# Kernel tuning notes

Measured on AMD Instinct MI355X. Metric: run time of the kernel, lower is better.

## Reference

```python
import jax, jax.numpy as jnp
import numpy as np

B, N, DIN, DM, NH = 8, 2048, 256, 256, 4
DK = DM // NH


def setup_inputs() -> dict:
    key = jax.random.key(0)
    ks = jax.random.split(key, 8)
    x = jax.random.normal(ks[0], (B, N, DIN), dtype=jnp.float32)
    # contiguous valid ranges per sample (padding on both ends), matching
    # the module's assumption that torch.where(mask)[0][0]/[−1] define a span
    starts = jax.random.randint(ks[1], (B,), 0, N // 8)
    lens = jax.random.randint(ks[2], (B,), N // 2, N - N // 8)
    pos = jnp.arange(N)
    attention_mask = ((pos[None, :] >= starts[:, None])
                      & (pos[None, :] < starts[:, None] + lens[:, None])).astype(jnp.int32)
    s = 0.02
    Wq = jax.random.normal(ks[3], (DIN, DM), jnp.float32) * s
    Wk = jax.random.normal(ks[4], (DIN, DM), jnp.float32) * s
    Wv = jax.random.normal(ks[5], (DIN, DM), jnp.float32) * s
    Wo = jax.random.normal(ks[6], (DM, DM), jnp.float32) * s
    bq = jnp.zeros((DM,), jnp.float32)
    bk = jnp.zeros((DM,), jnp.float32)
    bv = jnp.zeros((DM,), jnp.float32)
    bo = jnp.zeros((DM,), jnp.float32)
    return {"x": x, "attention_mask": attention_mask,
            "Wq": Wq, "bq": bq, "Wk": Wk, "bk": bk,
            "Wv": Wv, "bv": bv, "Wo": Wo, "bo": bo}


def reference(x, attention_mask, Wq, bq, Wk, bk, Wv, bv, Wo, bo):
    b, n, _ = x.shape
    nh, dk = NH, DK
    scale = 1.0 / np.sqrt(dk)
    q = (x @ Wq + bq).reshape(b, n, nh, dk).transpose(0, 2, 1, 3)  # [b,h,n,dk]
    k = (x @ Wk + bk).reshape(b, n, nh, dk).transpose(0, 2, 1, 3)
    v = (x @ Wv + bv).reshape(b, n, nh, dk).transpose(0, 2, 1, 3)
    dist = jnp.einsum('bhid,bhjd->bhij', q, k) * scale  # [b,h,n,n]

    # Vectorized equivalent of the per-sample python-loop mask:
    # start = first True index; end = last True index (torch slice start:end
    # is EXCLUSIVE of the last valid position -- preserved faithfully).
    m = attention_mask.astype(bool)
    pos = jnp.arange(n)
    start = jnp.argmax(m, axis=1)                      # [b]
    end = n - 1 - jnp.argmax(m[:, ::-1], axis=1)       # [b] last True index
    valid = (pos[None, :] >= start[:, None]) & (pos[None, :] < end[:, None])  # [b,n]
    bias = jnp.where(valid[:, :, None] & valid[:, None, :], 0.0, -1e10)       # [b,n,n]

    dist = jax.nn.softmax(dist + bias[:, None, :, :], axis=-1)
    att = jnp.einsum('bhij,bhjd->bhid', dist, v)       # [b,h,n,dk]
    att = att.transpose(0, 2, 1, 3).reshape(b, n, nh * dk)
    return att @ Wo + bo
```

## Files before the change

kernel.cpp:

```cpp
#include <hip/hip_runtime.h>
#include <hip/hip_bf16.h>
#include <math.h>

namespace {
constexpr int Bb  = 8;
constexpr int Nn  = 2048;
constexpr int DIN_ = 256;
constexpr int DM_  = 256;
constexpr int NH_  = 4;
constexpr int DK_  = 64;
constexpr int BH_  = Bb * NH_;
constexpr float SCALE = 0.125f;
}

typedef __attribute__((ext_vector_type(8))) _Float16 half8;
typedef __attribute__((ext_vector_type(2))) __fp16 fp16x2;
typedef __attribute__((ext_vector_type(4))) float f32x4;

static __device__ __forceinline__ unsigned pkrtz_u32(float a, float b) {
    union { fp16x2 h; unsigned u; } u;
    u.h = __builtin_amdgcn_cvt_pkrtz(a, b);
    return u.u;
}

static __device__ __forceinline__ half8 h8_from_u32x4(unsigned w0, unsigned w1,
                                                      unsigned w2, unsigned w3) {
    union { unsigned u[4]; half8 h; } u;
    u.u[0] = w0; u.u[1] = w1; u.u[2] = w2; u.u[3] = w3;
    return u.h;
}

__global__ __launch_bounds__(256) void prep_kernel(
    const int* __restrict__ mask, int* __restrict__ bounds,
    float* __restrict__ cmsum,
    const float* __restrict__ W0, const float* __restrict__ W1,
    const float* __restrict__ W2, const float* __restrict__ W3,
    _Float16* __restrict__ T0, _Float16* __restrict__ T1,
    _Float16* __restrict__ T2, _Float16* __restrict__ T3)
{
    const int bid = blockIdx.x;
    const int tid = threadIdx.x;
    if (bid < 8) {
        cmsum[bid * 256 + tid] = 0.0f;
        const int b = bid;
        __shared__ int smin[256], smax[256];
        int lmin = Nn, lmax = -1;
        for (int i = tid; i < Nn; i += 256) {
            if (mask[b * Nn + i]) {
                if (i < lmin) lmin = i;
                if (i > lmax) lmax = i;
            }
        }
        smin[tid] = lmin; smax[tid] = lmax;
        __syncthreads();
        for (int s = 128; s > 0; s >>= 1) {
            if (tid < s) {
                smin[tid] = min(smin[tid], smin[tid + s]);
                smax[tid] = max(smax[tid], smax[tid + s]);
            }
            __syncthreads();
        }
        if (tid == 0) { bounds[b * 2] = smin[0]; bounds[b * 2 + 1] = smax[0]; }
    } else {
        const int lin = bid - 8;
        const int wsel = lin >> 6;
        const float* W; _Float16* T;
        switch (wsel) {
            case 0: W = W0; T = T0; break;
            case 1: W = W1; T = T1; break;
            case 2: W = W2; T = T2; break;
            default: W = W3; T = T3; break;
        }
        const int idx = (lin & 63) * 256 + tid;
        const int n = idx & 255;
        const int k0 = (idx >> 8) << 2;
        _Float16 h4[4];
        #pragma unroll
        for (int j = 0; j < 4; ++j) h4[j] = (_Float16)W[(size_t)(k0 + j) * 256 + n];
        *(uint2*)&T[(size_t)n * 256 + k0] = *(const uint2*)h4;
    }
}

__global__ __launch_bounds__(256) void qkv_mfma(
    const float* __restrict__ x,
    const _Float16* __restrict__ Wtq, const float* __restrict__ bq,
    const _Float16* __restrict__ Wtk, const float* __restrict__ bk,
    const _Float16* __restrict__ Wtv, const float* __restrict__ bv,
    _Float16* __restrict__ Qh, _Float16* __restrict__ Kh, _Float16* __restrict__ Vt,
    float* __restrict__ cmsum)
{
    const int zsel = blockIdx.y >> 2;
    const int n0 = (blockIdx.y & 3) * 64;
    const int m0 = blockIdx.x * 128;
    const _Float16* Wt; const float* bias;
    if (zsel == 0)      { Wt = Wtq; bias = bq; }
    else if (zsel == 1) { Wt = Wtk; bias = bk; }
    else                { Wt = Wtv; bias = bv; }

    const int tid = threadIdx.x;
    const int w = tid >> 6, lane = tid & 63;
    const int a = lane & 15, g = lane >> 4;
    const int b = m0 >> 11;

    __shared__ __align__(16) _Float16 As[128 * 64];
    __shared__ __align__(16) _Float16 Bs[64 * 64];

    f32x4 acc[4][2] = {{{0,0,0,0},{0,0,0,0}},{{0,0,0,0},{0,0,0,0}},
                       {{0,0,0,0},{0,0,0,0}},{{0,0,0,0},{0,0,0,0}}};

    for (int step = 0; step < 4; ++step) {
        const int k0 = step * 64;
        {
            const int rb = tid >> 3, fc = tid & 7;
            #pragma unroll
            for (int p = 0; p < 4; ++p) {
                const int row = p * 32 + rb;
                const float4 v0 = *(const float4*)&x[(size_t)(m0 + row) * 256 + k0 + fc * 8];
                const float4 v1 = *(const float4*)&x[(size_t)(m0 + row) * 256 + k0 + fc * 8 + 4];
                _Float16 h[8];
                h[0]=(_Float16)v0.x; h[1]=(_Float16)v0.y; h[2]=(_Float16)v0.z; h[3]=(_Float16)v0.w;
                h[4]=(_Float16)v1.x; h[5]=(_Float16)v1.y; h[6]=(_Float16)v1.z; h[7]=(_Float16)v1.w;
                const int byo = (fc * 16) ^ ((row & 7) << 4);
                *(uint4*)((char*)As + row * 128 + byo) = *(const uint4*)h;
            }
        }
        #pragma unroll
        for (int i = 0; i < 2; ++i) {
            const int f = 2 * w + i;
            const int rowl = f * 8 + (lane >> 3);
            const int byo = ((lane & 7) * 16) ^ ((rowl & 7) << 4);
            const char* src = (const char*)(Wt + (size_t)(n0 + rowl) * 256 + k0) + byo;
            __builtin_amdgcn_global_load_lds(
                (const __attribute__((address_space(1))) void*)src,
                (__attribute__((address_space(3))) void*)((char*)Bs + f * 1024), 16, 0, 0);
        }
        __syncthreads();

        #pragma unroll
        for (int kc = 0; kc < 2; ++kc) {
            half8 xf[2], wf[4];
            #pragma unroll
            for (int tt = 0; tt < 2; ++tt) {
                const int row = 32 * w + 16 * tt + a;
                const int byo = (kc * 64 + g * 16) ^ ((row & 7) << 4);
                xf[tt] = *(const half8*)((const char*)As + row * 128 + byo);
            }
            #pragma unroll
            for (int nf = 0; nf < 4; ++nf) {
                const int row = 16 * nf + a;
                const int byo = (kc * 64 + g * 16) ^ ((row & 7) << 4);
                wf[nf] = *(const half8*)((const char*)Bs + row * 128 + byo);
            }
            if (zsel < 2) {
                #pragma unroll
                for (int nf = 0; nf < 4; ++nf)
                    #pragma unroll
                    for (int tt = 0; tt < 2; ++tt)
                        acc[nf][tt] = __builtin_amdgcn_mfma_f32_16x16x32_f16(wf[nf], xf[tt], acc[nf][tt], 0,0,0);
            } else {
                #pragma unroll
                for (int nf = 0; nf < 4; ++nf)
                    #pragma unroll
                    for (int tt = 0; tt < 2; ++tt)
                        acc[nf][tt] = __builtin_amdgcn_mfma_f32_16x16x32_f16(xf[tt], wf[nf], acc[nf][tt], 0,0,0);
            }
        }
        __syncthreads();
    }

    if (zsel < 2) {
        _Float16* out = zsel ? Kh : Qh;
        #pragma unroll
        for (int nf = 0; nf < 4; ++nf) {
            const int nb = n0 + 16 * nf + 4 * g;
            const f32x4 bi = *(const f32x4*)&bias[nb];
            const int h = nb >> 6, dkb = nb & 63;
            #pragma unroll
            for (int tt = 0; tt < 2; ++tt) {
                const int tok = (m0 + 32 * w + 16 * tt + a) & 2047;
                const f32x4 d = acc[nf][tt];
                _Float16 q4[4];
                q4[0] = (_Float16)(d[0] + bi[0]);
                q4[1] = (_Float16)(d[1] + bi[1]);
                q4[2] = (_Float16)(d[2] + bi[2]);
                q4[3] = (_Float16)(d[3] + bi[3]);
                *(uint2*)&out[(((size_t)(b * NH_ + h)) * Nn + tok) * DK_ + dkb] = *(const uint2*)q4;
            }
        }
    } else {
        const int h = n0 >> 6;
        #pragma unroll
        for (int nf = 0; nf < 4; ++nf) {
            const int n = n0 + 16 * nf + a;
            const float bs = bias[n];
            const int dk = 16 * nf + a;
            float csum = 8.0f * bs;
            #pragma unroll
            for (int tt = 0; tt < 2; ++tt) {
                const int tokb = (m0 + 32 * w + 16 * tt + 4 * g) & 2047;
                const f32x4 d = acc[nf][tt];
                csum += d[0] + d[1] + d[2] + d[3];
                uint2 pk;
                pk.x = pkrtz_u32(d[0] + bs, d[1] + bs);
                pk.y = pkrtz_u32(d[2] + bs, d[3] + bs);
                *(uint2*)&Vt[(((size_t)(b * NH_ + h)) * DK_ + dk) * Nn + tokb] = pk;
            }
            csum += __shfl_xor(csum, 16, 64);
            csum += __shfl_xor(csum, 32, 64);
            if (g == 0)
                atomicAdd(&cmsum[(b * NH_ + h) * DK_ + dk], csum);
        }
    }
}

__global__ __launch_bounds__(256) void flash_mfma(
    const _Float16* __restrict__ Q, const _Float16* __restrict__ K,
    const _Float16* __restrict__ Vt, const int* __restrict__ bounds,
    _Float16* __restrict__ Oh, float* __restrict__ lw)
{
    const int bid = blockIdx.x;
    const int xcd = bid & 7;
    const int rest = bid >> 3;
    const int qb  = rest & 31;
    const int j   = (rest >> 5) & 3;
    const int s   = rest >> 7;
    const int bh  = j * 8 + xcd;
    const int b  = bh >> 2, h = bh & 3;
    const int q0 = qb * 64;
    const int tid  = threadIdx.x;
    const int w    = tid >> 6;
    const int lane = tid & 63;
    const int a = lane & 15, g = lane >> 4;
    const int start = bounds[2 * b], endv = bounds[2 * b + 1];

    if (q0 + 63 < start || q0 >= endv) return;

    __shared__ __align__(16) _Float16 kfr[2][8][512];
    __shared__ __align__(16) _Float16 vfr[2][8][512];

    const _Float16* Qb = Q  + (size_t)bh * Nn * DK_;
    const _Float16* Kb = K  + (size_t)bh * Nn * DK_;
    const _Float16* Vb = Vt + (size_t)bh * DK_ * Nn;

    const int qrow = q0 + 16 * w + a;
    const half8 qf0 = *(const half8*)&Qb[(size_t)qrow * DK_ + 8 * g];
    const half8 qf1 = *(const half8*)&Qb[(size_t)qrow * DK_ + 32 + 8 * g];

    float l_i = 0.0f;
    f32x4 o0 = {0.f,0.f,0.f,0.f}, o1 = {0.f,0.f,0.f,0.f};
    f32x4 o2 = {0.f,0.f,0.f,0.f}, o3 = {0.f,0.f,0.f,0.f};

#define STAGE(cbuf, kt_) do {                                                        \
        _Pragma("unroll")                                                            \
        for (int ff = 0; ff < 2; ++ff) {                                             \
            const int f  = 2 * w + ff;                                               \
            const int tt = f >> 1, cc = f & 1;                                       \
            const _Float16* ks = &Kb[(size_t)((kt_) + 16 * tt + a) * DK_ + 32 * cc + 8 * g]; \
            __builtin_amdgcn_global_load_lds(                                        \
                (const __attribute__((address_space(1))) void*)ks,                   \
                (__attribute__((address_space(3))) void*)&kfr[cbuf][f][0], 16, 0, 0);\
            const _Float16* vs = &Vb[(size_t)(16 * tt + a) * Nn + (kt_) + 32 * cc + 8 * g]; \
            __builtin_amdgcn_global_load_lds(                                        \
                (const __attribute__((address_space(1))) void*)vs,                   \
                (__attribute__((address_space(3))) void*)&vfr[cbuf][f][0], 16, 0, 0);\
        }                                                                            \
    } while (0)

    const int t0 = start >> 6, t1 = (endv + 63) >> 6;
    const int nt = t1 - t0;
    const int n0t = (nt + 1) >> 1;
    const int ts = (s == 0) ? t0 : t0 + n0t;
    const int te = (s == 0) ? t0 + n0t : t1;

    if (ts < te) {
        const int lo = ts * 64, hiend = te * 64;
        int c = 0;
        STAGE(0, lo);

        for (int kt = lo; kt < hiend; kt += 64) {
            const int nxt = kt + 64;
            if (nxt < hiend) {
                STAGE(c ^ 1, nxt);
                asm volatile("s_waitcnt vmcnt(4)" ::: "memory");
            } else {
                asm volatile("s_waitcnt vmcnt(0)" ::: "memory");
            }
            __builtin_amdgcn_s_barrier();

            const _Float16* kf = &kfr[c][0][0];
            const _Float16* vf = &vfr[c][0][0];

            f32x4 st0 = {0.f,0.f,0.f,0.f}, st1 = {0.f,0.f,0.f,0.f};
            f32x4 st2 = {0.f,0.f,0.f,0.f}, st3 = {0.f,0.f,0.f,0.f};
            __builtin_amdgcn_s_setprio(1);
            st0 = __builtin_amdgcn_mfma_f32_16x16x32_f16(*(const half8*)&kf[0*512 + lane*8], qf0, st0, 0,0,0);
            st0 = __builtin_amdgcn_mfma_f32_16x16x32_f16(*(const half8*)&kf[1*512 + lane*8], qf1, st0, 0,0,0);
            st1 = __builtin_amdgcn_mfma_f32_16x16x32_f16(*(const half8*)&kf[2*512 + lane*8], qf0, st1, 0,0,0);
            st1 = __builtin_amdgcn_mfma_f32_16x16x32_f16(*(const half8*)&kf[3*512 + lane*8], qf1, st1, 0,0,0);
            st2 = __builtin_amdgcn_mfma_f32_16x16x32_f16(*(const half8*)&kf[4*512 + lane*8], qf0, st2, 0,0,0);
            st2 = __builtin_amdgcn_mfma_f32_16x16x32_f16(*(const half8*)&kf[5*512 + lane*8], qf1, st2, 0,0,0);
            st3 = __builtin_amdgcn_mfma_f32_16x16x32_f16(*(const half8*)&kf[6*512 + lane*8], qf0, st3, 0,0,0);
            st3 = __builtin_amdgcn_mfma_f32_16x16x32_f16(*(const half8*)&kf[7*512 + lane*8], qf1, st3, 0,0,0);
            __builtin_amdgcn_s_setprio(0);

            float pv[4][4];
            float rsum = 0.0f;
            const bool edge = (kt < start) || (kt + 64 > endv);
            if (edge) {
                #pragma unroll
                for (int t = 0; t < 4; ++t) {
                    const f32x4 sv = (t == 0) ? st0 : (t == 1) ? st1 : (t == 2) ? st2 : st3;
                    #pragma unroll
                    for (int r = 0; r < 4; ++r) {
                        const int col = kt + 16 * t + 4 * g + r;
                        const bool ok = (col >= start) && (col < endv);
                        const float e = ok ? __expf(sv[r] * SCALE) : 0.0f;
                        pv[t][r] = e;
                        rsum += e;
                    }
                }
            } else {
                #pragma unroll
                for (int t = 0; t < 4; ++t) {
                    const f32x4 sv = (t == 0) ? st0 : (t == 1) ? st1 : (t == 2) ? st2 : st3;
                    #pragma unroll
                    for (int r = 0; r < 4; ++r) {
                        const float e = __expf(sv[r] * SCALE);
                        pv[t][r] = e;
                        rsum += e;
                    }
                }
            }
            rsum += __shfl_xor(rsum, 16, 64);
            rsum += __shfl_xor(rsum, 32, 64);
            l_i += rsum;

            unsigned pk[4][2];
            #pragma unroll
            for (int t = 0; t < 4; ++t) {
                pk[t][0] = pkrtz_u32(pv[t][0], pv[t][1]);
                pk[t][1] = pkrtz_u32(pv[t][2], pv[t][3]);
            }
            const int gsel = g >> 1;
            unsigned aw[2][4];
            #pragma unroll
            for (int cq = 0; cq < 2; ++cq) {
                #pragma unroll
                for (int wd = 0; wd < 4; ++wd) {
                    const int srcLane = a + 16 * (2 * (g & 1) + (wd >> 1));
                    const int lo2 = __shfl((int)pk[2 * cq    ][wd & 1], srcLane, 64);
                    const int hi2 = __shfl((int)pk[2 * cq + 1][wd & 1], srcLane, 64);
                    aw[cq][wd] = (unsigned)(gsel ? hi2 : lo2);
                }
            }
            const half8 pa0 = h8_from_u32x4(aw[0][0], aw[0][1], aw[0][2], aw[0][3]);
            const half8 pa1 = h8_from_u32x4(aw[1][0], aw[1][1], aw[1][2], aw[1][3]);

            __builtin_amdgcn_s_setprio(1);
            o0 = __builtin_amdgcn_mfma_f32_16x16x32_f16(pa0, *(const half8*)&vf[0*512 + lane*8], o0, 0,0,0);
            o0 = __builtin_amdgcn_mfma_f32_16x16x32_f16(pa1, *(const half8*)&vf[1*512 + lane*8], o0, 0,0,0);
            o1 = __builtin_amdgcn_mfma_f32_16x16x32_f16(pa0, *(const half8*)&vf[2*512 + lane*8], o1, 0,0,0);
            o1 = __builtin_amdgcn_mfma_f32_16x16x32_f16(pa1, *(const half8*)&vf[3*512 + lane*8], o1, 0,0,0);
            o2 = __builtin_amdgcn_mfma_f32_16x16x32_f16(pa0, *(const half8*)&vf[4*512 + lane*8], o2, 0,0,0);
            o2 = __builtin_amdgcn_mfma_f32_16x16x32_f16(pa1, *(const half8*)&vf[5*512 + lane*8], o2, 0,0,0);
            o3 = __builtin_amdgcn_mfma_f32_16x16x32_f16(pa0, *(const half8*)&vf[6*512 + lane*8], o3, 0,0,0);
            o3 = __builtin_amdgcn_mfma_f32_16x16x32_f16(pa1, *(const half8*)&vf[7*512 + lane*8], o3, 0,0,0);
            __builtin_amdgcn_s_setprio(0);

            asm volatile("" ::: "memory");
            __builtin_amdgcn_s_barrier();
            c ^= 1;
        }
    }
#undef STAGE

    const size_t half = (size_t)Bb * Nn * DM_;
    _Float16* ob = Oh + (size_t)s * half + ((size_t)b * Nn) * DM_ + h * DK_;
    #pragma unroll
    for (int td = 0; td < 4; ++td) {
        const f32x4 ov = (td == 0) ? o0 : (td == 1) ? o1 : (td == 2) ? o2 : o3;
        #pragma unroll
        for (int r = 0; r < 4; ++r) {
            const int qr = q0 + 16 * w + 4 * g + r;
            ob[(size_t)qr * DM_ + 16 * td + a] = (_Float16)ov[r];
        }
    }
    if (g == 0) {
        const int tok = q0 + 16 * w + a;
        lw[(size_t)s * BH_ * Nn + (size_t)bh * Nn + tok] = l_i;
    }
}

__global__ __launch_bounds__(256) void proj_mfma(
    const _Float16* __restrict__ Oh, const float* __restrict__ lw,
    const int* __restrict__ bounds, const float* __restrict__ cmsum,
    const _Float16* __restrict__ Wt, const float* __restrict__ bias,
    float* __restrict__ out)
{
    const int m0 = blockIdx.x * 128;
    const int n0 = blockIdx.y * 64;
    const int tid = threadIdx.x;
    const int w = tid >> 6, lane = tid & 63;
    const int a = lane & 15, g = lane >> 4;
    const int b = m0 >> 11;
    const int start = bounds[2 * b], endv = bounds[2 * b + 1];

    __shared__ __align__(16) _Float16 As[128 * 64];
    __shared__ __align__(16) _Float16 Bs[64 * 64];

    const size_t half = (size_t)Bb * Nn * DM_;

    f32x4 acc[2][4] = {{{0,0,0,0},{0,0,0,0},{0,0,0,0},{0,0,0,0}},
                       {{0,0,0,0},{0,0,0,0},{0,0,0,0},{0,0,0,0}}};

    for (int step = 0; step < 4; ++step) {
        const int k0 = step * 64;
        {
            const int rb = tid >> 3, fc = tid & 7;
            #pragma unroll
            for (int p = 0; p < 4; ++p) {
                const int row = p * 32 + rb;
                const int tok = (m0 + row) & 2047;
                const bool valid = (tok >= start) && (tok < endv);
                const size_t rowoff = ((size_t)b * Nn + tok) * DM_ + k0 + fc * 8;
                _Float16 h[8];
                if (valid) {
                    const int bh = b * NH_ + step;
                    const float l0 = lw[(size_t)bh * Nn + tok];
                    const float l1 = lw[(size_t)BH_ * Nn + (size_t)bh * Nn + tok];
                    const float inv = 1.0f / (l0 + l1);
                    half8 a0 = *(const half8*)&Oh[rowoff];
                    half8 a1 = *(const half8*)&Oh[half + rowoff];
                    #pragma unroll
                    for (int k = 0; k < 8; ++k)
                        h[k] = (_Float16)(((float)a0[k] + (float)a1[k]) * inv);
                } else {
                    const float* cmp = &cmsum[(b * NH_ + step) * DK_ + fc * 8];
                    const float4 c0 = *(const float4*)cmp;
                    const float4 c1 = *(const float4*)(cmp + 4);
                    h[0]=(_Float16)(c0.x*(1.0f/2048.0f)); h[1]=(_Float16)(c0.y*(1.0f/2048.0f));
                    h[2]=(_Float16)(c0.z*(1.0f/2048.0f)); h[3]=(_Float16)(c0.w*(1.0f/2048.0f));
                    h[4]=(_Float16)(c1.x*(1.0f/2048.0f)); h[5]=(_Float16)(c1.y*(1.0f/2048.0f));
                    h[6]=(_Float16)(c1.z*(1.0f/2048.0f)); h[7]=(_Float16)(c1.w*(1.0f/2048.0f));
                }
                const int byo = (fc * 16) ^ ((row & 7) << 4);
                *(uint4*)((char*)As + row * 128 + byo) = *(const uint4*)h;
            }
        }
        #pragma unroll
        for (int i = 0; i < 2; ++i) {
            const int f = 2 * w + i;
            const int rowl = f * 8 + (lane >> 3);
            const int byo = ((lane & 7) * 16) ^ ((rowl & 7) << 4);
            const char* src = (const char*)(Wt + (size_t)(n0 + rowl) * 256 + k0) + byo;
            __builtin_amdgcn_global_load_lds(
                (const __attribute__((address_space(1))) void*)src,
                (__attribute__((address_space(3))) void*)((char*)Bs + f * 1024), 16, 0, 0);
        }
        __syncthreads();

        #pragma unroll
        for (int kc = 0; kc < 2; ++kc) {
            half8 af[2], wf[4];
            #pragma unroll
            for (int tt = 0; tt < 2; ++tt) {
                const int row = 32 * w + 16 * tt + a;
                const int byo = (kc * 64 + g * 16) ^ ((row & 7) << 4);
                af[tt] = *(const half8*)((const char*)As + row * 128 + byo);
            }
            #pragma unroll
            for (int nf = 0; nf < 4; ++nf) {
                const int row = 16 * nf + a;
                const int byo = (kc * 64 + g * 16) ^ ((row & 7) << 4);
                wf[nf] = *(const half8*)((const char*)Bs + row * 128 + byo);
            }
            #pragma unroll
            for (int tt = 0; tt < 2; ++tt)
                #pragma unroll
                for (int nf = 0; nf < 4; ++nf)
                    acc[tt][nf] = __builtin_amdgcn_mfma_f32_16x16x32_f16(af[tt], wf[nf], acc[tt][nf], 0,0,0);
        }
        __syncthreads();
    }

    #pragma unroll
    for (int tt = 0; tt < 2; ++tt) {
        #pragma unroll
        for (int nf = 0; nf < 4; ++nf) {
            const int n = n0 + 16 * nf + a;
            const float bs = bias[n];
            const f32x4 d = acc[tt][nf];
            const int mrow = m0 + 32 * w + 16 * tt + 4 * g;
            #pragma unroll
            for (int r = 0; r < 4; ++r)
                out[(size_t)(mrow + r) * 256 + n] = d[r] + bs;
        }
    }
}

extern "C" void kernel_launch(void* const* d_in, const int* in_sizes, int n_in,
                              void* d_out, int out_size, void* d_ws, size_t ws_size,
                              hipStream_t stream)
{
    const float* x    = (const float*)d_in[0];
    const int*   mask = (const int*)d_in[1];
    const float* Wq   = (const float*)d_in[2];
    const float* bq   = (const float*)d_in[3];
    const float* Wk   = (const float*)d_in[4];
    const float* bk   = (const float*)d_in[5];
    const float* Wv   = (const float*)d_in[6];
    const float* bv   = (const float*)d_in[7];
    const float* Wo   = (const float*)d_in[8];
    const float* bo   = (const float*)d_in[9];
    float* out = (float*)d_out;

    char* ws = (char*)d_ws;
    size_t off = 0;
    int* bounds = (int*)ws;                 off += 256;
    float* cmsum = (float*)(ws + off);      off += (size_t)BH_ * DK_ * sizeof(float);
    off = (off + 255) & ~(size_t)255;
    float* lw   = (float*)(ws + off);       off += (size_t)2 * BH_ * Nn * sizeof(float);
    const size_t h16_bytes = (size_t)BH_ * Nn * DK_ * sizeof(_Float16);
    _Float16* Qh  = (_Float16*)(ws + off); off += h16_bytes;
    _Float16* Kh  = (_Float16*)(ws + off); off += h16_bytes;
    _Float16* Vt  = (_Float16*)(ws + off); off += h16_bytes;
    _Float16* Oh  = (_Float16*)(ws + off); off += 2 * h16_bytes;
    _Float16* Wtq = (_Float16*)(ws + off); off += 256 * 256 * sizeof(_Float16);
    _Float16* Wtk = (_Float16*)(ws + off); off += 256 * 256 * sizeof(_Float16);
    _Float16* Wtv = (_Float16*)(ws + off); off += 256 * 256 * sizeof(_Float16);
    _Float16* Wto = (_Float16*)(ws + off); off += 256 * 256 * sizeof(_Float16);

    prep_kernel<<<264, 256, 0, stream>>>(mask, bounds, cmsum, Wq, Wk, Wv, Wo,
                                         Wtq, Wtk, Wtv, Wto);

    dim3 g1(128, 12);
    qkv_mfma<<<g1, 256, 0, stream>>>(x, Wtq, bq, Wtk, bk, Wtv, bv,
                                     Qh, Kh, Vt, cmsum);

    flash_mfma<<<2048, 256, 0, stream>>>(Qh, Kh, Vt, bounds, Oh, lw);

    dim3 g3(128, 4);
    proj_mfma<<<g3, 256, 0, stream>>>(Oh, lw, bounds, cmsum, Wto, bo, out);
}
```

Before: 168.7 us.

## Load K/V tiles directly into registers instead of LDS double-buffering

Replaces the shared-memory double-buffered K/V staging and its block barriers with per-wave direct global loads into registers. K for the next tile is prefetched into a ping-pong register array while V is loaded at the start of each tile. This removes LDS traffic and barriers but has each of the four waves load the same K/V data separately, raising global/L2 traffic and register pressure, and V load latency is no longer hidden.

Result: slower. 267.5 us (+58.5%).

```diff
diff --git a/kernel.cpp b/kernel.cpp
--- a/kernel.cpp
+++ b/kernel.cpp
@@ -235,9 +235,6 @@
 
     if (q0 + 63 < start || q0 >= endv) return;
 
-    __shared__ __align__(16) _Float16 kfr[2][8][512];
-    __shared__ __align__(16) _Float16 vfr[2][8][512];
-
     const _Float16* Qb = Q  + (size_t)bh * Nn * DK_;
     const _Float16* Kb = K  + (size_t)bh * Nn * DK_;
     const _Float16* Vb = Vt + (size_t)bh * DK_ * Nn;
@@ -249,22 +246,6 @@
     float l_i = 0.0f;
     f32x4 o0 = {0.f,0.f,0.f,0.f}, o1 = {0.f,0.f,0.f,0.f};
     f32x4 o2 = {0.f,0.f,0.f,0.f}, o3 = {0.f,0.f,0.f,0.f};
-
-#define STAGE(cbuf, kt_) do {                                                        \
-        _Pragma("unroll")                                                            \
-        for (int ff = 0; ff < 2; ++ff) {                                             \
-            const int f  = 2 * w + ff;                                               \
-            const int tt = f >> 1, cc = f & 1;                                       \
-            const _Float16* ks = &Kb[(size_t)((kt_) + 16 * tt + a) * DK_ + 32 * cc + 8 * g]; \
-            __builtin_amdgcn_global_load_lds(                                        \
-                (const __attribute__((address_space(1))) void*)ks,                   \
-                (__attribute__((address_space(3))) void*)&kfr[cbuf][f][0], 16, 0, 0);\
-            const _Float16* vs = &Vb[(size_t)(16 * tt + a) * Nn + (kt_) + 32 * cc + 8 * g]; \
-            __builtin_amdgcn_global_load_lds(                                        \
-                (const __attribute__((address_space(1))) void*)vs,                   \
-                (__attribute__((address_space(3))) void*)&vfr[cbuf][f][0], 16, 0, 0);\
-        }                                                                            \
-    } while (0)
 
     const int t0 = start >> 6, t1 = (endv + 63) >> 6;
     const int nt = t1 - t0;
@@ -274,105 +255,111 @@
 
     if (ts < te) {
         const int lo = ts * 64, hiend = te * 64;
-        int c = 0;
-        STAGE(0, lo);
-
-        for (int kt = lo; kt < hiend; kt += 64) {
-            const int nxt = kt + 64;
-            if (nxt < hiend) {
-                STAGE(c ^ 1, nxt);
-                asm volatile("s_waitcnt vmcnt(4)" ::: "memory");
-            } else {
-                asm volatile("s_waitcnt vmcnt(0)" ::: "memory");
-            }
-            __builtin_amdgcn_s_barrier();
-
-            const _Float16* kf = &kfr[c][0][0];
-            const _Float16* vf = &vfr[c][0][0];
-
-            f32x4 st0 = {0.f,0.f,0.f,0.f}, st1 = {0.f,0.f,0.f,0.f};
-            f32x4 st2 = {0.f,0.f,0.f,0.f}, st3 = {0.f,0.f,0.f,0.f};
-            __builtin_amdgcn_s_setprio(1);
-            st0 = __builtin_amdgcn_mfma_f32_16x16x32_f16(*(const half8*)&kf[0*512 + lane*8], qf0, st0, 0,0,0);
-            st0 = __builtin_amdgcn_mfma_f32_16x16x32_f16(*(const half8*)&kf[1*512 + lane*8], qf1, st0, 0,0,0);
-            st1 = __builtin_amdgcn_mfma_f32_16x16x32_f16(*(const half8*)&kf[2*512 + lane*8], qf0, st1, 0,0,0);
-            st1 = __builtin_amdgcn_mfma_f32_16x16x32_f16(*(const half8*)&kf[3*512 + lane*8], qf1, st1, 0,0,0);
-            st2 = __builtin_amdgcn_mfma_f32_16x16x32_f16(*(const half8*)&kf[4*512 + lane*8], qf0, st2, 0,0,0);
-            st2 = __builtin_amdgcn_mfma_f32_16x16x32_f16(*(const half8*)&kf[5*512 + lane*8], qf1, st2, 0,0,0);
-            st3 = __builtin_amdgcn_mfma_f32_16x16x32_f16(*(const half8*)&kf[6*512 + lane*8], qf0, st3, 0,0,0);
-            st3 = __builtin_amdgcn_mfma_f32_16x16x32_f16(*(const half8*)&kf[7*512 + lane*8], qf1, st3, 0,0,0);
-            __builtin_amdgcn_s_setprio(0);
-
-            float pv[4][4];
-            float rsum = 0.0f;
-            const bool edge = (kt < start) || (kt + 64 > endv);
-            if (edge) {
-                #pragma unroll
-                for (int t = 0; t < 4; ++t) {
-                    const f32x4 sv = (t == 0) ? st0 : (t == 1) ? st1 : (t == 2) ? st2 : st3;
-                    #pragma unroll
-                    for (int r = 0; r < 4; ++r) {
-                        const int col = kt + 16 * t + 4 * g + r;
-                        const bool ok = (col >= start) && (col < endv);
-                        const float e = ok ? __expf(sv[r] * SCALE) : 0.0f;
-                        pv[t][r] = e;
-                        rsum += e;
-                    }
-                }
-            } else {
-                #pragma unroll
-                for (int t = 0; t < 4; ++t) {
-                    const f32x4 sv = (t == 0) ? st0 : (t == 1) ? st1 : (t == 2) ? st2 : st3;
-                    #pragma unroll
-                    for (int r = 0; r < 4; ++r) {
-                        const float e = __expf(sv[r] * SCALE);
-                        pv[t][r] = e;
-                        rsum += e;
-                    }
-                }
-            }
-            rsum += __shfl_xor(rsum, 16, 64);
-            rsum += __shfl_xor(rsum, 32, 64);
-            l_i += rsum;
-
-            unsigned pk[4][2];
-            #pragma unroll
-            for (int t = 0; t < 4; ++t) {
-                pk[t][0] = pkrtz_u32(pv[t][0], pv[t][1]);
-                pk[t][1] = pkrtz_u32(pv[t][2], pv[t][3]);
-            }
-            const int gsel = g >> 1;
-            unsigned aw[2][4];
-            #pragma unroll
-            for (int cq = 0; cq < 2; ++cq) {
-                #pragma unroll
-                for (int wd = 0; wd < 4; ++wd) {
-                    const int srcLane = a + 16 * (2 * (g & 1) + (wd >> 1));
-                    const int lo2 = __shfl((int)pk[2 * cq    ][wd & 1], srcLane, 64);
-                    const int hi2 = __shfl((int)pk[2 * cq + 1][wd & 1], srcLane, 64);
-                    aw[cq][wd] = (unsigned)(gsel ? hi2 : lo2);
-                }
-            }
-            const half8 pa0 = h8_from_u32x4(aw[0][0], aw[0][1], aw[0][2], aw[0][3]);
-            const half8 pa1 = h8_from_u32x4(aw[1][0], aw[1][1], aw[1][2], aw[1][3]);
-
-            __builtin_amdgcn_s_setprio(1);
-            o0 = __builtin_amdgcn_mfma_f32_16x16x32_f16(pa0, *(const half8*)&vf[0*512 + lane*8], o0, 0,0,0);
-            o0 = __builtin_amdgcn_mfma_f32_16x16x32_f16(pa1, *(const half8*)&vf[1*512 + lane*8], o0, 0,0,0);
-            o1 = __builtin_amdgcn_mfma_f32_16x16x32_f16(pa0, *(const half8*)&vf[2*512 + lane*8], o1, 0,0,0);
-            o1 = __builtin_amdgcn_mfma_f32_16x16x32_f16(pa1, *(const half8*)&vf[3*512 + lane*8], o1, 0,0,0);
-            o2 = __builtin_amdgcn_mfma_f32_16x16x32_f16(pa0, *(const half8*)&vf[4*512 + lane*8], o2, 0,0,0);
-            o2 = __builtin_amdgcn_mfma_f32_16x16x32_f16(pa1, *(const half8*)&vf[5*512 + lane*8], o2, 0,0,0);
-            o3 = __builtin_amdgcn_mfma_f32_16x16x32_f16(pa0, *(const half8*)&vf[6*512 + lane*8], o3, 0,0,0);
-            o3 = __builtin_amdgcn_mfma_f32_16x16x32_f16(pa1, *(const half8*)&vf[7*512 + lane*8], o3, 0,0,0);
-            __builtin_amdgcn_s_setprio(0);
-
-            asm volatile("" ::: "memory");
-            __builtin_amdgcn_s_barrier();
-            c ^= 1;
-        }
-    }
-#undef STAGE
+
+#define LOADK(DST, KT) do {                                                          \
+        _Pragma("unroll")                                                            \
+        for (int f = 0; f < 8; ++f)                                                  \
+            DST[f] = *(const half8*)&Kb[(size_t)((KT) + 16 * (f >> 1) + a) * DK_     \
+                                        + 32 * (f & 1) + 8 * g];                     \
+    } while (0)
+
+#define TILE(KCUR, KNXT, KT) do {                                                    \
+        half8 vv[8];                                                                 \
+        _Pragma("unroll")                                                            \
+        for (int f = 0; f < 8; ++f)                                                  \
+            vv[f] = *(const half8*)&Vb[(size_t)(16 * (f >> 1) + a) * Nn + (KT)       \
+                                       + 32 * (f & 1) + 8 * g];                      \
+        f32x4 st0 = {0.f,0.f,0.f,0.f}, st1 = {0.f,0.f,0.f,0.f};                      \
+        f32x4 st2 = {0.f,0.f,0.f,0.f}, st3 = {0.f,0.f,0.f,0.f};                      \
+        __builtin_amdgcn_s_setprio(1);                                               \
+        st0 = __builtin_amdgcn_mfma_f32_16x16x32_f16(KCUR[0], qf0, st0, 0,0,0);      \
+        st0 = __builtin_amdgcn_mfma_f32_16x16x32_f16(KCUR[1], qf1, st0, 0,0,0);      \
+        st1 = __builtin_amdgcn_mfma_f32_16x16x32_f16(KCUR[2], qf0, st1, 0,0,0);      \
+        st1 = __builtin_amdgcn_mfma_f32_16x16x32_f16(KCUR[3], qf1, st1, 0,0,0);      \
+        st2 = __builtin_amdgcn_mfma_f32_16x16x32_f16(KCUR[4], qf0, st2, 0,0,0);      \
+        st2 = __builtin_amdgcn_mfma_f32_16x16x32_f16(KCUR[5], qf1, st2, 0,0,0);      \
+        st3 = __builtin_amdgcn_mfma_f32_16x16x32_f16(KCUR[6], qf0, st3, 0,0,0);      \
+        st3 = __builtin_amdgcn_mfma_f32_16x16x32_f16(KCUR[7], qf1, st3, 0,0,0);      \
+        __builtin_amdgcn_s_setprio(0);                                               \
+        const int ktn = ((KT) + 64 < hiend) ? (KT) + 64 : (KT);                      \
+        LOADK(KNXT, ktn);                                                            \
+        float pv[4][4];                                                              \
+        float rsum = 0.0f;                                                           \
+        const bool edge = ((KT) < start) || ((KT) + 64 > endv);                      \
+        if (edge) {                                                                  \
+            _Pragma("unroll")                                                        \
+            for (int t = 0; t < 4; ++t) {                                            \
+                const f32x4 sv = (t == 0) ? st0 : (t == 1) ? st1 : (t == 2) ? st2 : st3; \
+                _Pragma("unroll")                                                    \
+                for (int r = 0; r < 4; ++r) {                                        \
+                    const int col = (KT) + 16 * t + 4 * g + r;                       \
+                    const bool ok = (col >= start) && (col < endv);                  \
+                    const float e = ok ? __expf(sv[r] * SCALE) : 0.0f;               \
+                    pv[t][r] = e;                                                    \
+                    rsum += e;                                                       \
+                }                                                                    \
+            }                                                                        \
+        } else {                                                                     \
+            _Pragma("unroll")                                                        \
+            for (int t = 0; t < 4; ++t) {                                            \
+                const f32x4 sv = (t == 0) ? st0 : (t == 1) ? st1 : (t == 2) ? st2 : st3; \
+                _Pragma("unroll")                                                    \
+                for (int r = 0; r < 4; ++r) {                                        \
+                    const float e = __expf(sv[r] * SCALE);                           \
+                    pv[t][r] = e;                                                    \
+                    rsum += e;                                                       \
+                }                                                                    \
+            }                                                                        \
+        }                                                                            \
+        rsum += __shfl_xor(rsum, 16, 64);                                            \
+        rsum += __shfl_xor(rsum, 32, 64);                                            \
+        l_i += rsum;                                                                 \
+        unsigned pk[4][2];                                                           \
+        _Pragma("unroll")                                                            \
+        for (int t = 0; t < 4; ++t) {                                                \
+            pk[t][0] = pkrtz_u32(pv[t][0], pv[t][1]);                                \
+            pk[t][1] = pkrtz_u32(pv[t][2], pv[t][3]);                                \
+        }                                                                            \
+        const int gsel = g >> 1;                                                     \
+        unsigned aw[2][4];                                                           \
+        _Pragma("unroll")                                                            \
+        for (int cq = 0; cq < 2; ++cq) {                                             \
+            _Pragma("unroll")                                                        \
+            for (int wd = 0; wd < 4; ++wd) {                                         \
+                const int srcLane = a + 16 * (2 * (g & 1) + (wd >> 1));              \
+                const int lo2 = __shfl((int)pk[2 * cq    ][wd & 1], srcLane, 64);    \
+                const int hi2 = __shfl((int)pk[2 * cq + 1][wd & 1], srcLane, 64);    \
+                aw[cq][wd] = (unsigned)(gsel ? hi2 : lo2);                           \
+            }                                                                        \
+        }                                                                            \
+        const half8 pa0 = h8_from_u32x4(aw[0][0], aw[0][1], aw[0][2], aw[0][3]);     \
+        const half8 pa1 = h8_from_u32x4(aw[1][0], aw[1][1], aw[1][2], aw[1][3]);     \
+        __builtin_amdgcn_s_setprio(1);                                               \
+        o0 = __builtin_amdgcn_mfma_f32_16x16x32_f16(pa0, vv[0], o0, 0,0,0);          \
+        o0 = __builtin_amdgcn_mfma_f32_16x16x32_f16(pa1, vv[1], o0, 0,0,0);          \
+        o1 = __builtin_amdgcn_mfma_f32_16x16x32_f16(pa0, vv[2], o1, 0,0,0);          \
+        o1 = __builtin_amdgcn_mfma_f32_16x16x32_f16(pa1, vv[3], o1, 0,0,0);          \
+        o2 = __builtin_amdgcn_mfma_f32_16x16x32_f16(pa0, vv[4], o2, 0,0,0);          \
+        o2 = __builtin_amdgcn_mfma_f32_16x16x32_f16(pa1, vv[5], o2, 0,0,0);          \
+        o3 = __builtin_amdgcn_mfma_f32_16x16x32_f16(pa0, vv[6], o3, 0,0,0);          \
+        o3 = __builtin_amdgcn_mfma_f32_16x16x32_f16(pa1, vv[7], o3, 0,0,0);          \
+        __builtin_amdgcn_s_setprio(0);                                               \
+    } while (0)
+
+        half8 ka[8], kb2[8];
+        LOADK(ka, lo);
+        int kt = lo;
+        for (;;) {
+            TILE(ka, kb2, kt);
+            kt += 64;
+            if (kt >= hiend) break;
+            TILE(kb2, ka, kt);
+            kt += 64;
+            if (kt >= hiend) break;
+        }
+#undef TILE
+#undef LOADK
+    }
 
     const size_t half = (size_t)Bb * Nn * DM_;
     _Float16* ob = Oh + (size_t)s * half + ((size_t)b * Nn) * DM_ + h * DK_;
```
